# Kernel optimization log

Hardware: AMD Instinct MI355X
Metric: run time of the kernel (lower is better)

Reference implementation:

```python
import jax, jax.numpy as jnp
import numpy as np

N = 800000      # octree nodes at this depth
CIN = 32
COUT = 64
K = 27          # 3x3x3 kernel neighborhood
EPS = 1e-5
GROUPS = COUT // 4


def group_norm(x, w, b, groups=GROUPS, eps=EPS):
    # x: [N, C]; per-node GroupNorm over channel groups (torch GroupNorm on [N, C])
    n, c = x.shape
    xg = x.reshape(n, groups, c // groups)
    mu = jnp.mean(xg, axis=-1, keepdims=True)
    var = jnp.mean(jnp.square(xg - mu), axis=-1, keepdims=True)
    xn = (xg - mu) * jax.lax.rsqrt(var + eps)
    return xn.reshape(n, c) * w + b


def octree_conv(x, neigh, W):
    # x: [N, Cin], neigh: [N, K] int, W: [K, Cin, Cout]
    # out[i] = sum_k x[neigh[i, k]] @ W[k]; fixed small loop over K kernel taps
    out = x[neigh[:, 0]] @ W[0]
    for k in range(1, W.shape[0]):
        out = out + x[neigh[:, k]] @ W[k]
    return out


def setup_inputs() -> dict:
    key = jax.random.key(0)
    ks = jax.random.split(key, 12)
    data = jax.random.normal(ks[0], (N, CIN), jnp.float32)
    neigh = jax.random.randint(ks[1], (N, K), 0, N, dtype=jnp.int64)
    scale_a = 1.0 / np.sqrt(K * CIN)
    scale_b = 1.0 / np.sqrt(K * COUT)
    Wa = jax.random.normal(ks[2], (K, CIN, COUT), jnp.float32) * scale_a
    Wb = jax.random.normal(ks[3], (K, COUT, COUT), jnp.float32) * scale_b
    W1 = jax.random.normal(ks[4], (CIN, COUT), jnp.float32) * (1.0 / np.sqrt(CIN))
    ga_w = 1.0 + 0.1 * jax.random.normal(ks[5], (COUT,), jnp.float32)
    ga_b = 0.01 * jax.random.normal(ks[6], (COUT,), jnp.float32)
    gb_w = 1.0 + 0.1 * jax.random.normal(ks[7], (COUT,), jnp.float32)
    gb_b = 0.01 * jax.random.normal(ks[8], (COUT,), jnp.float32)
    gs_w = 1.0 + 0.1 * jax.random.normal(ks[9], (COUT,), jnp.float32)
    gs_b = 0.01 * jax.random.normal(ks[10], (COUT,), jnp.float32)
    return {"data": data, "neigh": neigh, "Wa": Wa, "ga_w": ga_w, "ga_b": ga_b,
            "Wb": Wb, "gb_w": gb_w, "gb_b": gb_b, "W1": W1, "gs_w": gs_w, "gs_b": gs_b}


def reference(data, neigh, Wa, ga_w, ga_b, Wb, gb_w, gb_b, W1, gs_w, gs_b):
    # conv3x3a: OctreeConv -> GroupNorm -> ReLU
    h = jax.nn.relu(group_norm(octree_conv(data, neigh, Wa), ga_w, ga_b))
    # conv3x3b: OctreeConv -> GroupNorm
    h2 = group_norm(octree_conv(h, neigh, Wb), gb_w, gb_b)
    # shortcut (in_channels != out_channels): Conv1x1 -> GroupNorm
    sc = group_norm(data @ W1, gs_w, gs_b)
    return jax.nn.relu(h2 + sc)
```

## Files before the change

### kernel.cpp

```cpp
#include <hip/hip_runtime.h>

#define NNODES 800000
#define CINC   32
#define COUTC  64
#define KT     27
#define EPSV   1e-5f

typedef _Float16 half8 __attribute__((ext_vector_type(8)));
typedef _Float16 half4 __attribute__((ext_vector_type(4)));
typedef float    f32x4 __attribute__((ext_vector_type(4)));

#define MFMA(A, B, C) __builtin_amdgcn_mfma_f32_16x16x32_f16((A), (B), (C), 0, 0, 0)
#define SBAR()  __builtin_amdgcn_s_barrier()
#define SCHED() __builtin_amdgcn_sched_barrier(0)

__device__ __forceinline__ void gl2lds(const _Float16* g, _Float16* l) {
  __builtin_amdgcn_global_load_lds(
      (const __attribute__((address_space(1))) void*)g,
      (__attribute__((address_space(3))) void*)l, 16, 0, 0);
}

__device__ __forceinline__ f32x4 gn4(f32x4 v, const float* __restrict__ w,
                                     const float* __restrict__ b, int cb) {
  const float mu = (v[0] + v[1] + v[2] + v[3]) * 0.25f;
  f32x4 d;
#pragma unroll
  for (int j = 0; j < 4; ++j) d[j] = v[j] - mu;
  const float var = (d[0] * d[0] + d[1] * d[1] + d[2] * d[2] + d[3] * d[3]) * 0.25f;
  const float rs = 1.0f / sqrtf(var + EPSV);
  const f32x4 wv = *(const f32x4*)(w + cb);
  const f32x4 bv = *(const f32x4*)(b + cb);
  f32x4 r;
#pragma unroll
  for (int j = 0; j < 4; ++j) r[j] = d[j] * rs * wv[j] + bv[j];
  return r;
}

__global__ __launch_bounds__(256) void k_split(const float* __restrict__ x,
                                               _Float16* __restrict__ dpk, int n4) {
  const int i = blockIdx.x * 256 + threadIdx.x;
  if (i >= n4) return;
  const f32x4 v = ((const f32x4*)x)[i];
  half4 h, l;
#pragma unroll
  for (int j = 0; j < 4; ++j) {
    h[j] = (_Float16)v[j];
    l[j] = (_Float16)(v[j] - (float)h[j]);
  }
  const int n = i >> 3, g = i & 7;
  *(half4*)(dpk + (size_t)n * 64 + g * 4) = h;
  *(half4*)(dpk + (size_t)n * 64 + 32 + g * 4) = l;
}

__global__ __launch_bounds__(256) void k_prepw(const float* __restrict__ Wa,
                                               const float* __restrict__ Wb,
                                               const float* __restrict__ W1,
                                               _Float16* __restrict__ waT,
                                               _Float16* __restrict__ wbT,
                                               _Float16* __restrict__ w1T) {
  const int u = blockIdx.x * 256 + threadIdx.x;
  const float* s;
  _Float16* d;
  size_t db;
  int cin0, cout;
  if (u < 6912) {
    const int tap = u >> 8, r = u & 255, t = r >> 6, l = r & 63;
    cin0 = (l >> 4) * 8;
    cout = t * 16 + (l & 15);
    s = Wa + (size_t)tap * CINC * COUTC;
    d = waT;
    db = ((size_t)(tap * 8 + t * 2) * 64 + l) * 8;
  } else if (u < 20736) {
    const int u2 = u - 6912;
    const int tap = u2 >> 9, r = u2 & 511, t = r >> 7, r2 = r & 127;
    const int kc = r2 >> 6, l = r2 & 63;
    cin0 = kc * 32 + (l >> 4) * 8;
    cout = t * 16 + (l & 15);
    s = Wb + (size_t)tap * COUTC * COUTC;
    d = wbT;
    db = ((size_t)(tap * 16 + t * 4 + kc * 2) * 64 + l) * 8;
  } else if (u < 20992) {
    const int u3 = u - 20736, t = u3 >> 6, l = u3 & 63;
    cin0 = (l >> 4) * 8;
    cout = t * 16 + (l & 15);
    s = W1;
    d = w1T;
    db = ((size_t)(t * 2) * 64 + l) * 8;
  } else {
    return;
  }
  half8 h, l8;
#pragma unroll
  for (int j = 0; j < 8; ++j) {
    const float v = s[(size_t)(cin0 + j) * COUTC + cout];
    h[j] = (_Float16)v;
    l8[j] = (_Float16)(v - (float)h[j]);
  }
  *(half8*)(d + db) = h;
  *(half8*)(d + db + 512) = l8;
}

#define STAGEA(T, SL)                                                          \
  {                                                                            \
    const _Float16* sp_ = waT + (size_t)(T)*4096 + (wave * 2) * 512 + lane * 8;\
    _Float16* dp_ = s_w + (SL)*4096 + (wave * 2) * 512;                        \
    gl2lds(sp_, dp_);                                                          \
    gl2lds(sp_ + 512, dp_ + 512);                                              \
  }

#define GATHA(T, GB)                                                           \
  {                                                                            \
    const int i0_ = s_n[ln0 * KT + (T)];                                       \
    const int i1_ = s_n[(ln0 + 16) * KT + (T)];                                \
    const _Float16* p0_ = dpk + (size_t)i0_ * 64 + q * 8;                      \
    const _Float16* p1_ = dpk + (size_t)i1_ * 64 + q * 8;                      \
    GB[0] = *(const half8*)(p0_);                                              \
    GB[1] = *(const half8*)(p0_ + 32);                                         \
    GB[2] = *(const half8*)(p1_);                                              \
    GB[3] = *(const half8*)(p1_ + 32);                                         \
  }

#define STEPA(T, S, GBC, GBN, VMS, DOSTAGE, DOG)                               \
  {                                                                            \
    SCHED();                                                                   \
    SBAR();                           \
    SCHED();                                                                   \
    if (DOSTAGE) STAGEA((T) + 1, 1 - (S));                                     \
    if (DOG) GATHA((T) + 2, GBN);                                              \
    asm volatile("s_waitcnt vmcnt(" VMS ")" ::: "memory");                     \
    SCHED();                                                                   \
    SBAR();                         \
    SCHED();                                                                   \
    _Pragma("unroll") for (int t4 = 0; t4 < 4; ++t4) {                         \
      const _Float16* wb_ = s_w + (S)*4096 + (t4 * 2) * 512 + lane * 8;        \
      const half8 wh_ = *(const half8*)(wb_);                                  \
      const half8 wl_ = *(const half8*)(wb_ + 512);                            \
      acc[t4][0] = MFMA(wh_, GBC[0], acc[t4][0]);                              \
      acc[t4][0] = MFMA(wh_, GBC[1], acc[t4][0]);                              \
      acc[t4][0] = MFMA(wl_, GBC[0], acc[t4][0]);                              \
      acc[t4][1] = MFMA(wh_, GBC[2], acc[t4][1]);                              \
      acc[t4][1] = MFMA(wh_, GBC[3], acc[t4][1]);                              \
      acc[t4][1] = MFMA(wl_, GBC[2], acc[t4][1]);                              \
    }                                                                          \
  }

__global__ __launch_bounds__(256, 4) void k_conva(
    const _Float16* __restrict__ dpk, const int* __restrict__ neigh,
    const _Float16* __restrict__ waT, const float* __restrict__ gw,
    const float* __restrict__ gb, _Float16* __restrict__ hpk) {
  __shared__ int s_n[128 * KT];
  __shared__ _Float16 s_w[2 * 4096];
  const int tid = threadIdx.x;
  const int wave = tid >> 6, lane = tid & 63;
  const int cl = lane & 15, q = lane >> 4;
  const int node0 = blockIdx.x * 128;

  for (int j = tid; j < 128 * KT; j += 256) s_n[j] = neigh[(size_t)node0 * KT + j];
  __syncthreads();

  f32x4 acc[4][2] = {};
  const int ln0 = wave * 32 + cl;
  half8 g0[4], g1[4], g2[4];

  STAGEA(0, 0);
  GATHA(0, g0);
  GATHA(1, g1);

  for (int c6 = 0; c6 < 24; c6 += 6) {
    STEPA(c6 + 0, 0, g0, g2, "10", 1, 1);
    STEPA(c6 + 1, 1, g1, g0, "10", 1, 1);
    STEPA(c6 + 2, 0, g2, g1, "10", 1, 1);
    STEPA(c6 + 3, 1, g0, g2, "10", 1, 1);
    STEPA(c6 + 4, 0, g1, g0, "10", 1, 1);
    STEPA(c6 + 5, 1, g2, g1, "10", 1, 1);
  }
  STEPA(24, 0, g0, g2, "10", 1, 1);
  STEPA(25, 1, g1, g0, "6", 1, 0);
  STEPA(26, 0, g2, g1, "0", 0, 0);

#pragma unroll
  for (int t = 0; t < 4; ++t)
#pragma unroll
    for (int nt = 0; nt < 2; ++nt) {
      const int node = node0 + wave * 32 + nt * 16 + cl;
      const int cb = t * 16 + q * 4;
      const f32x4 g = gn4(acc[t][nt], gw, gb, cb);
      half4 h, l;
#pragma unroll
      for (int j = 0; j < 4; ++j) {
        const float v = fmaxf(g[j], 0.0f);
        h[j] = (_Float16)v;
        l[j] = (_Float16)(v - (float)h[j]);
      }
      *(half4*)(hpk + (size_t)node * 128 + cb) = h;
      *(half4*)(hpk + (size_t)node * 128 + 64 + cb) = l;
    }
}

#define STAGEB(T, SL)                                                          \
  {                                                                            \
    const _Float16* sp_ = wbT + (size_t)(T)*8192 + (wave * 4) * 512 + lane * 8;\
    _Float16* dp_ = s_w + (SL)*8192 + (wave * 4) * 512;                        \
    gl2lds(sp_, dp_);                                                          \
    gl2lds(sp_ + 512, dp_ + 512);                                              \
    gl2lds(sp_ + 1024, dp_ + 1024);                                            \
    gl2lds(sp_ + 1536, dp_ + 1536);                                            \
  }

#define GATHB(T, GB)                                                           \
  {                                                                            \
    const int i0_ = s_n[ln0 * KT + (T)];                                       \
    const int i1_ = s_n[(ln0 + 16) * KT + (T)];                                \
    const _Float16* p0_ = hpk + (size_t)i0_ * 128 + q * 8;                     \
    const _Float16* p1_ = hpk + (size_t)i1_ * 128 + q * 8;                     \
    GB[0] = *(const half8*)(p0_);                                              \
    GB[1] = *(const half8*)(p0_ + 32);                                         \
    GB[2] = *(const half8*)(p0_ + 64);                                         \
    GB[3] = *(const half8*)(p0_ + 96);                                         \
    GB[4] = *(const half8*)(p1_);                                              \
    GB[5] = *(const half8*)(p1_ + 32);                                         \
    GB[6] = *(const half8*)(p1_ + 64);                                         \
    GB[7] = *(const half8*)(p1_ + 96);                                         \
  }

#define STEPB(T, S, GBC, GBN, VMS, DOSTAGE, DOG)                               \
  {                                                                            \
    SCHED();                                                                   \
    SBAR();                                                                    \
    SCHED();                                                                   \
    if (DOSTAGE) STAGEB((T) + 1, 1 - (S));                                     \
    if (DOG) GATHB((T) + 2, GBN);                                              \
    asm volatile("s_waitcnt vmcnt(" VMS ")" ::: "memory");                     \
    SCHED();                                                                   \
    SBAR();                                                                    \
    SCHED();                                                                   \
    _Pragma("unroll") for (int t4 = 0; t4 < 4; ++t4) {                         \
      const _Float16* wb_ = s_w + (S)*8192 + (t4 * 4) * 512 + lane * 8;        \
      const half8 wha_ = *(const half8*)(wb_);                                 \
      const half8 wla_ = *(const half8*)(wb_ + 512);                           \
      const half8 whb_ = *(const half8*)(wb_ + 1024);                          \
      const half8 wlb_ = *(const half8*)(wb_ + 1536);                          \
      acc[t4][0] = MFMA(wha_, GBC[0], acc[t4][0]);                             \
      acc[t4][0] = MFMA(wha_, GBC[2], acc[t4][0]);                             \
      acc[t4][0] = MFMA(wla_, GBC[0], acc[t4][0]);                             \
      acc[t4][0] = MFMA(whb_, GBC[1], acc[t4][0]);                             \
      acc[t4][0] = MFMA(whb_, GBC[3], acc[t4][0]);                             \
      acc[t4][0] = MFMA(wlb_, GBC[1], acc[t4][0]);                             \
      acc[t4][1] = MFMA(wha_, GBC[4], acc[t4][1]);                             \
      acc[t4][1] = MFMA(wha_, GBC[6], acc[t4][1]);                             \
      acc[t4][1] = MFMA(wla_, GBC[4], acc[t4][1]);                             \
      acc[t4][1] = MFMA(whb_, GBC[5], acc[t4][1]);                             \
      acc[t4][1] = MFMA(whb_, GBC[7], acc[t4][1]);                             \
      acc[t4][1] = MFMA(wlb_, GBC[5], acc[t4][1]);                             \
    }                                                                          \
  }

__global__ __launch_bounds__(256, 3) void k_convb(
    const _Float16* __restrict__ hpk, const _Float16* __restrict__ dpk,
    const int* __restrict__ neigh, const _Float16* __restrict__ wbT,
    const _Float16* __restrict__ w1T,
    const float* __restrict__ gbw, const float* __restrict__ gbb,
    const float* __restrict__ gsw, const float* __restrict__ gsb,
    float* __restrict__ out) {
  __shared__ int s_n[128 * KT];
  __shared__ _Float16 s_w[2 * 8192];
  const int tid = threadIdx.x;
  const int wave = tid >> 6, lane = tid & 63;
  const int cl = lane & 15, q = lane >> 4;
  const int node0 = blockIdx.x * 128;

  for (int j = tid; j < 128 * KT; j += 256) s_n[j] = neigh[(size_t)node0 * KT + j];
  __syncthreads();

  f32x4 acc[4][2] = {};
  const int ln0 = wave * 32 + cl;
  half8 g0[8], g1[8], g2[8];

  STAGEB(0, 0);
  GATHB(0, g0);
  GATHB(1, g1);

  for (int c6 = 0; c6 < 24; c6 += 6) {
    STEPB(c6 + 0, 0, g0, g2, "20", 1, 1);
    STEPB(c6 + 1, 1, g1, g0, "20", 1, 1);
    STEPB(c6 + 2, 0, g2, g1, "20", 1, 1);
    STEPB(c6 + 3, 1, g0, g2, "20", 1, 1);
    STEPB(c6 + 4, 0, g1, g0, "20", 1, 1);
    STEPB(c6 + 5, 1, g2, g1, "20", 1, 1);
  }
  STEPB(24, 0, g0, g2, "20", 1, 1);
  STEPB(25, 1, g1, g0, "12", 1, 0);
  STEPB(26, 0, g2, g1, "0", 0, 0);

  f32x4 sc[4][2] = {};
  {
    const int n0g = node0 + wave * 32 + cl;
    const _Float16* p0 = dpk + (size_t)n0g * 64 + q * 8;
    const _Float16* p1 = dpk + (size_t)(n0g + 16) * 64 + q * 8;
    const half8 sh0 = *(const half8*)(p0);
    const half8 sl0 = *(const half8*)(p0 + 32);
    const half8 sh1 = *(const half8*)(p1);
    const half8 sl1 = *(const half8*)(p1 + 32);
    const _Float16* w1p = w1T + lane * 8;
#pragma unroll
    for (int t = 0; t < 4; ++t) {
      const half8 wh = *(const half8*)(w1p + (size_t)(t * 2) * 512);
      const half8 wl = *(const half8*)(w1p + (size_t)(t * 2) * 512 + 512);
      sc[t][0] = MFMA(wh, sh0, sc[t][0]);
      sc[t][0] = MFMA(wh, sl0, sc[t][0]);
      sc[t][0] = MFMA(wl, sh0, sc[t][0]);
      sc[t][1] = MFMA(wh, sh1, sc[t][1]);
      sc[t][1] = MFMA(wh, sl1, sc[t][1]);
      sc[t][1] = MFMA(wl, sh1, sc[t][1]);
    }
  }

#pragma unroll
  for (int t = 0; t < 4; ++t)
#pragma unroll
    for (int nt = 0; nt < 2; ++nt) {
      const int node = node0 + wave * 32 + nt * 16 + cl;
      const int cb = t * 16 + q * 4;
      const f32x4 a = gn4(acc[t][nt], gbw, gbb, cb);
      const f32x4 s = gn4(sc[t][nt], gsw, gsb, cb);
      f32x4 o;
#pragma unroll
      for (int j = 0; j < 4; ++j) o[j] = fmaxf(a[j] + s[j], 0.0f);
      *(f32x4*)(out + (size_t)node * 64 + cb) = o;
    }
}

extern "C" void kernel_launch(void* const* d_in, const int* in_sizes, int n_in,
                              void* d_out, int out_size, void* d_ws, size_t ws_size,
                              hipStream_t stream) {
  const float* data = (const float*)d_in[0];
  const int* neigh = (const int*)d_in[1];
  const float* Wa = (const float*)d_in[2];
  const float* gaw = (const float*)d_in[3];
  const float* gab = (const float*)d_in[4];
  const float* Wb = (const float*)d_in[5];
  const float* gbw = (const float*)d_in[6];
  const float* gbb = (const float*)d_in[7];
  const float* W1 = (const float*)d_in[8];
  const float* gsw = (const float*)d_in[9];
  const float* gsb = (const float*)d_in[10];
  float* out = (float*)d_out;

  char* ws = (char*)d_ws;
  _Float16* dpk = (_Float16*)(ws);
  _Float16* hpk = (_Float16*)(ws + 102400000);
  _Float16* waT = (_Float16*)(ws + 307200000);
  _Float16* wbT = (_Float16*)(ws + 307421184);
  _Float16* w1T = (_Float16*)(ws + 307863552);

  k_split<<<25000, 256, 0, stream>>>(data, dpk, NNODES * CINC / 4);
  k_prepw<<<82, 256, 0, stream>>>(Wa, Wb, W1, waT, wbT, w1T);

  k_conva<<<NNODES / 128, 256, 0, stream>>>(dpk, neigh, waT, gaw, gab, hpk);
  k_convb<<<NNODES / 128, 256, 0, stream>>>(hpk, dpk, neigh, wbT, w1T,
                                            gbw, gbb, gsw, gsb, out);
}
```

Baseline: 1.606 ms.

## Split hi/lo activation buffers and run two gather passes in convb; triple-buffer conva

The intermediate activation is now stored as two separate planar buffers (high and low fp16 parts) instead of one interleaved 128-wide row. k_convb runs the 27-tap gather loop twice: first over the high part with the full weight split, then over the low part with only the high weights, so each pass gathers a 64-element row. This shrinks per-step register and gather footprint but reads the neighbor indices and weights a second time. k_conva moves to a three-slot weight stage and four gather buffers, prefetching one step further ahead, which costs extra LDS and registers.

```diff
diff --git a/kernel.cpp b/kernel.cpp
--- a/kernel.cpp
+++ b/kernel.cpp
@@ -120,19 +120,19 @@
     GB[3] = *(const half8*)(p1_ + 32);                                         \
   }
 
-#define STEPA(T, S, GBC, GBN, VMS, DOSTAGE, DOG)                               \
-  {                                                                            \
-    SCHED();                                                                   \
-    SBAR();                           \
-    SCHED();                                                                   \
-    if (DOSTAGE) STAGEA((T) + 1, 1 - (S));                                     \
-    if (DOG) GATHA((T) + 2, GBN);                                              \
+#define STEPA(T, RS, WS, GBC, GBN, VMS, DOSTAGE, DOG)                          \
+  {                                                                            \
+    SCHED();                                                                   \
+    SBAR();                                                                    \
+    SCHED();                                                                   \
+    if (DOSTAGE) STAGEA((T) + 2, WS);                                          \
+    if (DOG) GATHA((T) + 3, GBN);                                              \
     asm volatile("s_waitcnt vmcnt(" VMS ")" ::: "memory");                     \
     SCHED();                                                                   \
-    SBAR();                         \
+    SBAR();                                                                    \
     SCHED();                                                                   \
     _Pragma("unroll") for (int t4 = 0; t4 < 4; ++t4) {                         \
-      const _Float16* wb_ = s_w + (S)*4096 + (t4 * 2) * 512 + lane * 8;        \
+      const _Float16* wb_ = s_w + (RS)*4096 + (t4 * 2) * 512 + lane * 8;       \
       const half8 wh_ = *(const half8*)(wb_);                                  \
       const half8 wl_ = *(const half8*)(wb_ + 512);                            \
       acc[t4][0] = MFMA(wh_, GBC[0], acc[t4][0]);                              \
@@ -147,9 +147,10 @@
 __global__ __launch_bounds__(256, 4) void k_conva(
     const _Float16* __restrict__ dpk, const int* __restrict__ neigh,
     const _Float16* __restrict__ waT, const float* __restrict__ gw,
-    const float* __restrict__ gb, _Float16* __restrict__ hpk) {
+    const float* __restrict__ gb, _Float16* __restrict__ hhi,
+    _Float16* __restrict__ hlo) {
   __shared__ int s_n[128 * KT];
-  __shared__ _Float16 s_w[2 * 4096];
+  __shared__ _Float16 s_w[3 * 4096];
   const int tid = threadIdx.x;
   const int wave = tid >> 6, lane = tid & 63;
   const int cl = lane & 15, q = lane >> 4;
@@ -160,23 +161,41 @@
 
   f32x4 acc[4][2] = {};
   const int ln0 = wave * 32 + cl;
-  half8 g0[4], g1[4], g2[4];
+  half8 g0[4], g1[4], g2[4], g3[4];
 
   STAGEA(0, 0);
+  STAGEA(1, 1);
   GATHA(0, g0);
   GATHA(1, g1);
-
-  for (int c6 = 0; c6 < 24; c6 += 6) {
-    STEPA(c6 + 0, 0, g0, g2, "10", 1, 1);
-    STEPA(c6 + 1, 1, g1, g0, "10", 1, 1);
-    STEPA(c6 + 2, 0, g2, g1, "10", 1, 1);
-    STEPA(c6 + 3, 1, g0, g2, "10", 1, 1);
-    STEPA(c6 + 4, 0, g1, g0, "10", 1, 1);
-    STEPA(c6 + 5, 1, g2, g1, "10", 1, 1);
-  }
-  STEPA(24, 0, g0, g2, "10", 1, 1);
-  STEPA(25, 1, g1, g0, "6", 1, 0);
-  STEPA(26, 0, g2, g1, "0", 0, 0);
+  GATHA(2, g2);
+
+  STEPA(0, 0, 2, g0, g3, "14", 1, 1);
+  STEPA(1, 1, 0, g1, g0, "16", 1, 1);
+  STEPA(2, 2, 1, g2, g1, "16", 1, 1);
+  STEPA(3, 0, 2, g3, g2, "16", 1, 1);
+  STEPA(4, 1, 0, g0, g3, "16", 1, 1);
+  STEPA(5, 2, 1, g1, g0, "16", 1, 1);
+  STEPA(6, 0, 2, g2, g1, "16", 1, 1);
+  STEPA(7, 1, 0, g3, g2, "16", 1, 1);
+  STEPA(8, 2, 1, g0, g3, "16", 1, 1);
+  STEPA(9, 0, 2, g1, g0, "16", 1, 1);
+  STEPA(10, 1, 0, g2, g1, "16", 1, 1);
+  STEPA(11, 2, 1, g3, g2, "16", 1, 1);
+  STEPA(12, 0, 2, g0, g3, "16", 1, 1);
+  STEPA(13, 1, 0, g1, g0, "16", 1, 1);
+  STEPA(14, 2, 1, g2, g1, "16", 1, 1);
+  STEPA(15, 0, 2, g3, g2, "16", 1, 1);
+  STEPA(16, 1, 0, g0, g3, "16", 1, 1);
+  STEPA(17, 2, 1, g1, g0, "16", 1, 1);
+  STEPA(18, 0, 2, g2, g1, "16", 1, 1);
+  STEPA(19, 1, 0, g3, g2, "16", 1, 1);
+  STEPA(20, 2, 1, g0, g3, "16", 1, 1);
+  STEPA(21, 0, 2, g1, g0, "16", 1, 1);
+  STEPA(22, 1, 0, g2, g1, "16", 1, 1);
+  STEPA(23, 2, 1, g3, g2, "16", 1, 1);
+  STEPA(24, 0, 2, g0, g3, "12", 1, 0);
+  STEPA(25, 1, 0, g1, g0, "6", 0, 0);
+  STEPA(26, 2, 1, g2, g1, "0", 0, 0);
 
 #pragma unroll
   for (int t = 0; t < 4; ++t)
@@ -192,12 +211,12 @@
         h[j] = (_Float16)v;
         l[j] = (_Float16)(v - (float)h[j]);
       }
-      *(half4*)(hpk + (size_t)node * 128 + cb) = h;
-      *(half4*)(hpk + (size_t)node * 128 + 64 + cb) = l;
+      *(half4*)(hhi + (size_t)node * 64 + cb) = h;
+      *(half4*)(hlo + (size_t)node * 64 + cb) = l;
     }
 }
 
-#define STAGEB(T, SL)                                                          \
+#define STAGEH(T, SL)                                                          \
   {                                                                            \
     const _Float16* sp_ = wbT + (size_t)(T)*8192 + (wave * 4) * 512 + lane * 8;\
     _Float16* dp_ = s_w + (SL)*8192 + (wave * 4) * 512;                        \
@@ -207,29 +226,25 @@
     gl2lds(sp_ + 1536, dp_ + 1536);                                            \
   }
 
-#define GATHB(T, GB)                                                           \
+#define GATHH(T, GB)                                                           \
   {                                                                            \
     const int i0_ = s_n[ln0 * KT + (T)];                                       \
     const int i1_ = s_n[(ln0 + 16) * KT + (T)];                                \
-    const _Float16* p0_ = hpk + (size_t)i0_ * 128 + q * 8;                     \
-    const _Float16* p1_ = hpk + (size_t)i1_ * 128 + q * 8;                     \
+    const _Float16* p0_ = hhi + (size_t)i0_ * 64 + q * 8;                      \
+    const _Float16* p1_ = hhi + (size_t)i1_ * 64 + q * 8;                      \
     GB[0] = *(const half8*)(p0_);                                              \
     GB[1] = *(const half8*)(p0_ + 32);                                         \
-    GB[2] = *(const half8*)(p0_ + 64);                                         \
-    GB[3] = *(const half8*)(p0_ + 96);                                         \
-    GB[4] = *(const half8*)(p1_);                                              \
-    GB[5] = *(const half8*)(p1_ + 32);                                         \
-    GB[6] = *(const half8*)(p1_ + 64);                                         \
-    GB[7] = *(const half8*)(p1_ + 96);                                         \
-  }
-
-#define STEPB(T, S, GBC, GBN, VMS, DOSTAGE, DOG)                               \
-  {                                                                            \
-    SCHED();                                                                   \
-    SBAR();                                                                    \
-    SCHED();                                                                   \
-    if (DOSTAGE) STAGEB((T) + 1, 1 - (S));                                     \
-    if (DOG) GATHB((T) + 2, GBN);                                              \
+    GB[2] = *(const half8*)(p1_);                                              \
+    GB[3] = *(const half8*)(p1_ + 32);                                         \
+  }
+
+#define STEPH(T, S, GBC, GBN, VMS, DOSTAGE, DOG)                               \
+  {                                                                            \
+    SCHED();                                                                   \
+    SBAR();                                                                    \
+    SCHED();                                                                   \
+    if (DOSTAGE) STAGEH((T) + 1, 1 - (S));                                     \
+    if (DOG) GATHH((T) + 2, GBN);                                              \
     asm volatile("s_waitcnt vmcnt(" VMS ")" ::: "memory");                     \
     SCHED();                                                                   \
     SBAR();                                                                    \
@@ -241,24 +256,62 @@
       const half8 whb_ = *(const half8*)(wb_ + 1024);                          \
       const half8 wlb_ = *(const half8*)(wb_ + 1536);                          \
       acc[t4][0] = MFMA(wha_, GBC[0], acc[t4][0]);                             \
-      acc[t4][0] = MFMA(wha_, GBC[2], acc[t4][0]);                             \
       acc[t4][0] = MFMA(wla_, GBC[0], acc[t4][0]);                             \
       acc[t4][0] = MFMA(whb_, GBC[1], acc[t4][0]);                             \
-      acc[t4][0] = MFMA(whb_, GBC[3], acc[t4][0]);                             \
       acc[t4][0] = MFMA(wlb_, GBC[1], acc[t4][0]);                             \
-      acc[t4][1] = MFMA(wha_, GBC[4], acc[t4][1]);                             \
-      acc[t4][1] = MFMA(wha_, GBC[6], acc[t4][1]);                             \
-      acc[t4][1] = MFMA(wla_, GBC[4], acc[t4][1]);                             \
-      acc[t4][1] = MFMA(whb_, GBC[5], acc[t4][1]);                             \
-      acc[t4][1] = MFMA(whb_, GBC[7], acc[t4][1]);                             \
-      acc[t4][1] = MFMA(wlb_, GBC[5], acc[t4][1]);                             \
+      acc[t4][1] = MFMA(wha_, GBC[2], acc[t4][1]);                             \
+      acc[t4][1] = MFMA(wla_, GBC[2], acc[t4][1]);                             \
+      acc[t4][1] = MFMA(whb_, GBC[3], acc[t4][1]);                             \
+      acc[t4][1] = MFMA(wlb_, GBC[3], acc[t4][1]);                             \
     }                                                                          \
   }
 
+#define STAGEL(T, SL)                                                          \
+  {                                                                            \
+    const _Float16* sp_ = wbT + (size_t)(T)*8192 + (wave * 4) * 512 + lane * 8;\
+    _Float16* dp_ = s_w + (SL)*4096 + (wave * 2) * 512;                        \
+    gl2lds(sp_, dp_);                                                          \
+    gl2lds(sp_ + 1024, dp_ + 512);                                             \
+  }
+
+#define GATHL(T, GB)                                                           \
+  {                                                                            \
+    const int i0_ = s_n[ln0 * KT + (T)];                                       \
+    const int i1_ = s_n[(ln0 + 16) * KT + (T)];                                \
+    const _Float16* p0_ = hlo + (size_t)i0_ * 64 + q * 8;                      \
+    const _Float16* p1_ = hlo + (size_t)i1_ * 64 + q * 8;                      \
+    GB[0] = *(const half8*)(p0_);                                              \
+    GB[1] = *(const half8*)(p0_ + 32);                                         \
+    GB[2] = *(const half8*)(p1_);                                              \
+    GB[3] = *(const half8*)(p1_ + 32);                                         \
+  }
+
+#define STEPL(T, S, GBC, GBN, VMS, DOSTAGE, DOG)                               \
+  {                                                                            \
+    SCHED();                                                                   \
+    SBAR();                                                                    \
+    SCHED();                                                                   \
+    if (DOSTAGE) STAGEL((T) + 1, 1 - (S));                                     \
+    if (DOG) GATHL((T) + 2, GBN);                                              \
+    asm volatile("s_waitcnt vmcnt(" VMS ")" ::: "memory");                     \
+    SCHED();                                                                   \
+    SBAR();                                                                    \
+    SCHED();                                                                   \
+    _Pragma("unroll") for (int t4 = 0; t4 < 4; ++t4) {                         \
+      const _Float16* wb_ = s_w + (S)*4096 + (t4 * 2) * 512 + lane * 8;        \
+      const half8 wha_ = *(const half8*)(wb_);                                 \
+      const half8 whb_ = *(const half8*)(wb_ + 512);                           \
+      acc[t4][0] = MFMA(wha_, GBC[0], acc[t4][0]);                             \
+      acc[t4][0] = MFMA(whb_, GBC[1], acc[t4][0]);                             \
+      acc[t4][1] = MFMA(wha_, GBC[2], acc[t4][1]);                             \
+      acc[t4][1] = MFMA(whb_, GBC[3], acc[t4][1]);                             \
+    }                                                                          \
+  }
+
 __global__ __launch_bounds__(256, 3) void k_convb(
-    const _Float16* __restrict__ hpk, const _Float16* __restrict__ dpk,
-    const int* __restrict__ neigh, const _Float16* __restrict__ wbT,
-    const _Float16* __restrict__ w1T,
+    const _Float16* __restrict__ hhi, const _Float16* __restrict__ hlo,
+    const _Float16* __restrict__ dpk, const int* __restrict__ neigh,
+    const _Float16* __restrict__ wbT, const _Float16* __restrict__ w1T,
     const float* __restrict__ gbw, const float* __restrict__ gbb,
     const float* __restrict__ gsw, const float* __restrict__ gsb,
     float* __restrict__ out) {
@@ -274,23 +327,40 @@
 
   f32x4 acc[4][2] = {};
   const int ln0 = wave * 32 + cl;
-  half8 g0[8], g1[8], g2[8];
-
-  STAGEB(0, 0);
-  GATHB(0, g0);
-  GATHB(1, g1);
-
+  half8 g0[4], g1[4], g2[4];
+
+  STAGEH(0, 0);
+  GATHH(0, g0);
+  GATHH(1, g1);
   for (int c6 = 0; c6 < 24; c6 += 6) {
-    STEPB(c6 + 0, 0, g0, g2, "20", 1, 1);
-    STEPB(c6 + 1, 1, g1, g0, "20", 1, 1);
-    STEPB(c6 + 2, 0, g2, g1, "20", 1, 1);
-    STEPB(c6 + 3, 1, g0, g2, "20", 1, 1);
-    STEPB(c6 + 4, 0, g1, g0, "20", 1, 1);
-    STEPB(c6 + 5, 1, g2, g1, "20", 1, 1);
-  }
-  STEPB(24, 0, g0, g2, "20", 1, 1);
-  STEPB(25, 1, g1, g0, "12", 1, 0);
-  STEPB(26, 0, g2, g1, "0", 0, 0);
+    STEPH(c6 + 0, 0, g0, g2, "12", 1, 1);
+    STEPH(c6 + 1, 1, g1, g0, "12", 1, 1);
+    STEPH(c6 + 2, 0, g2, g1, "12", 1, 1);
+    STEPH(c6 + 3, 1, g0, g2, "12", 1, 1);
+    STEPH(c6 + 4, 0, g1, g0, "12", 1, 1);
+    STEPH(c6 + 5, 1, g2, g1, "12", 1, 1);
+  }
+  STEPH(24, 0, g0, g2, "12", 1, 1);
+  STEPH(25, 1, g1, g0, "8", 1, 0);
+  STEPH(26, 0, g2, g1, "0", 0, 0);
+
+  SCHED();
+  SBAR();
+  SCHED();
+  STAGEL(0, 0);
+  GATHL(0, g0);
+  GATHL(1, g1);
+  for (int c6 = 0; c6 < 24; c6 += 6) {
+    STEPL(c6 + 0, 0, g0, g2, "10", 1, 1);
+    STEPL(c6 + 1, 1, g1, g0, "10", 1, 1);
+    STEPL(c6 + 2, 0, g2, g1, "10", 1, 1);
+    STEPL(c6 + 3, 1, g0, g2, "10", 1, 1);
+    STEPL(c6 + 4, 0, g1, g0, "10", 1, 1);
+    STEPL(c6 + 5, 1, g2, g1, "10", 1, 1);
+  }
+  STEPL(24, 0, g0, g2, "10", 1, 1);
+  STEPL(25, 1, g1, g0, "6", 1, 0);
+  STEPL(26, 0, g2, g1, "0", 0, 0);
 
   f32x4 sc[4][2] = {};
   {
@@ -348,7 +418,8 @@
 
   char* ws = (char*)d_ws;
   _Float16* dpk = (_Float16*)(ws);
-  _Float16* hpk = (_Float16*)(ws + 102400000);
+  _Float16* hhi = (_Float16*)(ws + 102400000);
+  _Float16* hlo = (_Float16*)(ws + 204800000);
   _Float16* waT = (_Float16*)(ws + 307200000);
   _Float16* wbT = (_Float16*)(ws + 307421184);
   _Float16* w1T = (_Float16*)(ws + 307863552);
@@ -356,7 +427,7 @@
   k_split<<<25000, 256, 0, stream>>>(data, dpk, NNODES * CINC / 4);
   k_prepw<<<82, 256, 0, stream>>>(Wa, Wb, W1, waT, wbT, w1T);
 
-  k_conva<<<NNODES / 128, 256, 0, stream>>>(dpk, neigh, waT, gaw, gab, hpk);
-  k_convb<<<NNODES / 128, 256, 0, stream>>>(hpk, dpk, neigh, wbT, w1T,
+  k_conva<<<NNODES / 128, 256, 0, stream>>>(dpk, neigh, waT, gaw, gab, hhi, hlo);
+  k_convb<<<NNODES / 128, 256, 0, stream>>>(hhi, hlo, dpk, neigh, wbT, w1T,
                                             gbw, gbb, gsw, gsb, out);
 }
```

New measurement: 1.827 ms. 13.8% more time.

## Deepen conva pipeline to triple-buffered weights and add nontemporal streaming accesses

Applied to the files above, without the earlier changes.

The first octree conv kernel moves from double to triple LDS weight buffering and from a two-tap to a three-tap register gather lookahead, so more gather loads are in flight per barrier step. The main loop is fully unrolled and the vmcnt wait thresholds are retuned to match. Separately, streaming loads and stores (input split, neighbor index loads, shortcut input, hpk and output writes) are made nontemporal to reduce cache pollution for the randomly gathered data. The change costs more registers and LDS in conva, which may lower occupancy, and the hand-set waitcnt values must stay correct.

```diff
diff --git a/kernel.cpp b/kernel.cpp
--- a/kernel.cpp
+++ b/kernel.cpp
@@ -13,6 +13,8 @@
 #define MFMA(A, B, C) __builtin_amdgcn_mfma_f32_16x16x32_f16((A), (B), (C), 0, 0, 0)
 #define SBAR()  __builtin_amdgcn_s_barrier()
 #define SCHED() __builtin_amdgcn_sched_barrier(0)
+#define NTL(p)     __builtin_nontemporal_load(p)
+#define NTS(v, p)  __builtin_nontemporal_store((v), (p))
 
 __device__ __forceinline__ void gl2lds(const _Float16* g, _Float16* l) {
   __builtin_amdgcn_global_load_lds(
@@ -40,7 +42,7 @@
                                                _Float16* __restrict__ dpk, int n4) {
   const int i = blockIdx.x * 256 + threadIdx.x;
   if (i >= n4) return;
-  const f32x4 v = ((const f32x4*)x)[i];
+  const f32x4 v = NTL(&((const f32x4*)x)[i]);
   half4 h, l;
 #pragma unroll
   for (int j = 0; j < 4; ++j) {
@@ -120,19 +122,19 @@
     GB[3] = *(const half8*)(p1_ + 32);                                         \
   }
 
-#define STEPA(T, S, GBC, GBN, VMS, DOSTAGE, DOG)                               \
-  {                                                                            \
-    SCHED();                                                                   \
-    SBAR();                           \
-    SCHED();                                                                   \
-    if (DOSTAGE) STAGEA((T) + 1, 1 - (S));                                     \
-    if (DOG) GATHA((T) + 2, GBN);                                              \
+#define STEPA(T, RS, WS, GBC, GBN, VMS, DOSTAGE, DOG)                          \
+  {                                                                            \
+    SCHED();                                                                   \
+    SBAR();                                                                    \
+    SCHED();                                                                   \
+    if (DOSTAGE) STAGEA((T) + 2, WS);                                          \
+    if (DOG) GATHA((T) + 3, GBN);                                              \
     asm volatile("s_waitcnt vmcnt(" VMS ")" ::: "memory");                     \
     SCHED();                                                                   \
-    SBAR();                         \
+    SBAR();                                                                    \
     SCHED();                                                                   \
     _Pragma("unroll") for (int t4 = 0; t4 < 4; ++t4) {                         \
-      const _Float16* wb_ = s_w + (S)*4096 + (t4 * 2) * 512 + lane * 8;        \
+      const _Float16* wb_ = s_w + (RS)*4096 + (t4 * 2) * 512 + lane * 8;       \
       const half8 wh_ = *(const half8*)(wb_);                                  \
       const half8 wl_ = *(const half8*)(wb_ + 512);                            \
       acc[t4][0] = MFMA(wh_, GBC[0], acc[t4][0]);                              \
@@ -149,34 +151,53 @@
     const _Float16* __restrict__ waT, const float* __restrict__ gw,
     const float* __restrict__ gb, _Float16* __restrict__ hpk) {
   __shared__ int s_n[128 * KT];
-  __shared__ _Float16 s_w[2 * 4096];
+  __shared__ _Float16 s_w[3 * 4096];
   const int tid = threadIdx.x;
   const int wave = tid >> 6, lane = tid & 63;
   const int cl = lane & 15, q = lane >> 4;
   const int node0 = blockIdx.x * 128;
 
-  for (int j = tid; j < 128 * KT; j += 256) s_n[j] = neigh[(size_t)node0 * KT + j];
+  for (int j = tid; j < 128 * KT; j += 256)
+    s_n[j] = NTL(&neigh[(size_t)node0 * KT + j]);
   __syncthreads();
 
   f32x4 acc[4][2] = {};
   const int ln0 = wave * 32 + cl;
-  half8 g0[4], g1[4], g2[4];
+  half8 g0[4], g1[4], g2[4], g3[4];
 
   STAGEA(0, 0);
+  STAGEA(1, 1);
   GATHA(0, g0);
   GATHA(1, g1);
-
-  for (int c6 = 0; c6 < 24; c6 += 6) {
-    STEPA(c6 + 0, 0, g0, g2, "10", 1, 1);
-    STEPA(c6 + 1, 1, g1, g0, "10", 1, 1);
-    STEPA(c6 + 2, 0, g2, g1, "10", 1, 1);
-    STEPA(c6 + 3, 1, g0, g2, "10", 1, 1);
-    STEPA(c6 + 4, 0, g1, g0, "10", 1, 1);
-    STEPA(c6 + 5, 1, g2, g1, "10", 1, 1);
-  }
-  STEPA(24, 0, g0, g2, "10", 1, 1);
-  STEPA(25, 1, g1, g0, "6", 1, 0);
-  STEPA(26, 0, g2, g1, "0", 0, 0);
+  GATHA(2, g2);
+
+  STEPA(0, 0, 2, g0, g3, "14", 1, 1);
+  STEPA(1, 1, 0, g1, g0, "16", 1, 1);
+  STEPA(2, 2, 1, g2, g1, "16", 1, 1);
+  STEPA(3, 0, 2, g3, g2, "16", 1, 1);
+  STEPA(4, 1, 0, g0, g3, "16", 1, 1);
+  STEPA(5, 2, 1, g1, g0, "16", 1, 1);
+  STEPA(6, 0, 2, g2, g1, "16", 1, 1);
+  STEPA(7, 1, 0, g3, g2, "16", 1, 1);
+  STEPA(8, 2, 1, g0, g3, "16", 1, 1);
+  STEPA(9, 0, 2, g1, g0, "16", 1, 1);
+  STEPA(10, 1, 0, g2, g1, "16", 1, 1);
+  STEPA(11, 2, 1, g3, g2, "16", 1, 1);
+  STEPA(12, 0, 2, g0, g3, "16", 1, 1);
+  STEPA(13, 1, 0, g1, g0, "16", 1, 1);
+  STEPA(14, 2, 1, g2, g1, "16", 1, 1);
+  STEPA(15, 0, 2, g3, g2, "16", 1, 1);
+  STEPA(16, 1, 0, g0, g3, "16", 1, 1);
+  STEPA(17, 2, 1, g1, g0, "16", 1, 1);
+  STEPA(18, 0, 2, g2, g1, "16", 1, 1);
+  STEPA(19, 1, 0, g3, g2, "16", 1, 1);
+  STEPA(20, 2, 1, g0, g3, "16", 1, 1);
+  STEPA(21, 0, 2, g1, g0, "16", 1, 1);
+  STEPA(22, 1, 0, g2, g1, "16", 1, 1);
+  STEPA(23, 2, 1, g3, g2, "16", 1, 1);
+  STEPA(24, 0, 2, g0, g3, "12", 1, 0);
+  STEPA(25, 1, 0, g1, g0, "6", 0, 0);
+  STEPA(26, 2, 1, g2, g1, "0", 0, 0);
 
 #pragma unroll
   for (int t = 0; t < 4; ++t)
@@ -192,8 +213,8 @@
         h[j] = (_Float16)v;
         l[j] = (_Float16)(v - (float)h[j]);
       }
-      *(half4*)(hpk + (size_t)node * 128 + cb) = h;
-      *(half4*)(hpk + (size_t)node * 128 + 64 + cb) = l;
+      NTS(h, (half4*)(hpk + (size_t)node * 128 + cb));
+      NTS(l, (half4*)(hpk + (size_t)node * 128 + 64 + cb));
     }
 }
 
@@ -269,7 +290,8 @@
   const int cl = lane & 15, q = lane >> 4;
   const int node0 = blockIdx.x * 128;
 
-  for (int j = tid; j < 128 * KT; j += 256) s_n[j] = neigh[(size_t)node0 * KT + j];
+  for (int j = tid; j < 128 * KT; j += 256)
+    s_n[j] = NTL(&neigh[(size_t)node0 * KT + j]);
   __syncthreads();
 
   f32x4 acc[4][2] = {};
@@ -297,10 +319,10 @@
     const int n0g = node0 + wave * 32 + cl;
     const _Float16* p0 = dpk + (size_t)n0g * 64 + q * 8;
     const _Float16* p1 = dpk + (size_t)(n0g + 16) * 64 + q * 8;
-    const half8 sh0 = *(const half8*)(p0);
-    const half8 sl0 = *(const half8*)(p0 + 32);
-    const half8 sh1 = *(const half8*)(p1);
-    const half8 sl1 = *(const half8*)(p1 + 32);
+    const half8 sh0 = NTL((const half8*)(p0));
+    const half8 sl0 = NTL((const half8*)(p0 + 32));
+    const half8 sh1 = NTL((const half8*)(p1));
+    const half8 sl1 = NTL((const half8*)(p1 + 32));
     const _Float16* w1p = w1T + lane * 8;
 #pragma unroll
     for (int t = 0; t < 4; ++t) {
@@ -326,7 +348,7 @@
       f32x4 o;
 #pragma unroll
       for (int j = 0; j < 4; ++j) o[j] = fmaxf(a[j] + s[j], 0.0f);
-      *(f32x4*)(out + (size_t)node * 64 + cb) = o;
+      NTS(o, (f32x4*)(out + (size_t)node * 64 + cb));
     }
 }
 
```

Result: no change. 1.615 ms (+0.6%).
